# Optimization experiments

Measured on AMD Instinct MI355X. Metric: run time of the kernel, lower is better.

The kernel has to match this reference:

```python
import jax, jax.numpy as jnp
import numpy as np

N, F, O, K = 4096, 128, 128, 4


def setup_inputs() -> dict:
    key = jax.random.key(0)
    ks = jax.random.split(key, 7)
    shift = jax.random.uniform(ks[0], (N, N), jnp.float32) * (1.0 / N)  # dense stand-in for sparse adjacency
    A2 = shift * shift  # elementwise square, as in torch.mul(all_A, all_A)
    x = jax.random.normal(ks[1], (N, F), jnp.float32)
    nan_mask = jax.random.bernoulli(ks[2], 0.1, (N, F))
    features = jnp.where(nan_mask, jnp.nan, x)
    limit = float(np.sqrt(6.0 / (F + O)))  # xavier_uniform
    weight = jax.random.uniform(ks[3], (F, O), jnp.float32, -limit, limit)
    pi = jnp.log(jax.nn.softmax(jax.random.normal(ks[4], (K,), jnp.float32)))  # log mixture weights
    mu = jax.random.normal(ks[5], (K, F), jnp.float32)  # GMM means
    sigma = jnp.log(jax.random.uniform(ks[6], (K, F), jnp.float32, minval=0.5, maxval=1.5))  # log diag covs
    return {"shift": shift, "features": features, "weight": weight,
            "pi": pi, "mu": mu, "sigma": sigma, "A2": A2}


def ex_relu(mu_t, sig_t):
    # E[relu(X)] for X ~ N(mu_t, sig_t), with exact relu fallback when variance == 0
    is_zero = sig_t == 0
    s = jnp.where(is_zero, 1e-10, sig_t)
    sqrt_s = jnp.sqrt(s)
    w = mu_t / sqrt_s
    inv_sqrt_2pi = 1.0 / np.sqrt(2.0 * np.pi)
    nr = sqrt_s * (jnp.exp(-0.5 * w * w) * inv_sqrt_2pi
                   + 0.5 * w * (1.0 + jax.lax.erf(w / np.sqrt(2.0))))
    return jnp.where(is_zero, jnp.maximum(mu_t, 0.0), nr)


def reference(shift, features, weight, pi, mu, sigma, A2):
    dim = features.shape[1]
    x_isnan = jnp.isnan(features)[None, :, :]            # [1, N, F] -> broadcasts over K
    variances = jnp.exp(sigma)                           # [K, F]
    # GMM imputation: mean/variance per component where features missing
    mean_mat = jnp.where(x_isnan, mu[:, None, :], features[None, :, :])      # [K, N, F]
    var_mat = jnp.where(x_isnan, variances[:, None, :], 0.0)                 # [K, N, F]
    # dense GEMMs
    transform_x = jnp.einsum('knf,fo->kno', mean_mat, weight)                # [K, N, O]
    transform_covs = jnp.einsum('knf,fo->kno', var_mat, weight * weight)     # [K, N, O]
    # K graph propagations (spmm in the original)
    conv_x = jnp.einsum('nm,kmo->kno', shift, transform_x)
    conv_covs = jnp.einsum('nm,kmo->kno', A2, transform_covs)
    expected_x = ex_relu(conv_x, conv_covs)                                  # [K, N, O]
    # responsibilities gamma: softmax over components of log pi + log N(x; mu, var)
    log_n = (-0.5 * jnp.sum((mean_mat - mu[:, None, :]) ** 2 / variances[:, None, :], axis=2)
             - 0.5 * dim * np.log(2.0 * np.pi) - 0.5 * jnp.sum(sigma))       # [K, N]
    gamma = jax.nn.softmax(pi[:, None] + log_n, axis=0)                      # [K, N]
    return jnp.sum(expected_x * gamma[:, :, None], axis=0)                   # [N, O]
```

## Files before the change

kernel.cpp:

```cpp
#include <hip/hip_runtime.h>


#define NN 4096
#define FF 128
#define KK 4

typedef _Float16 f16;
typedef f16 f16x8 __attribute__((ext_vector_type(8)));
typedef f16 f16x4 __attribute__((ext_vector_type(4)));
typedef float f32x4 __attribute__((ext_vector_type(4)));

typedef const __attribute__((address_space(1))) void* gptr1_t;
typedef __attribute__((address_space(3))) void* lptr3_t;

__device__ __forceinline__ void gload_lds16(const void* g, void* l) {
  __builtin_amdgcn_global_load_lds((gptr1_t)g, (lptr3_t)l, 16, 0, 0);
}

__device__ __forceinline__ bool is_nan_bits(float x) {
  return (__float_as_uint(x) & 0x7fffffffu) > 0x7f800000u;
}

__global__ __launch_bounds__(256) void k0_prep(
    const float* __restrict__ W, const float* __restrict__ mu,
    const float* __restrict__ sigma, f16* __restrict__ Wx, f16* __restrict__ Wc,
    f16* __restrict__ muh, f16* __restrict__ varh, float* __restrict__ invvar) {
  int tid = blockIdx.x * 256 + threadIdx.x;
  for (int i = tid; i < 16384; i += (int)gridDim.x * 256) {
    int j = i & 7;
    int o = (i >> 3) & 127;
    int g = (i >> 10) & 3;
    int fc = i >> 12;
    int f = fc * 32 + g * 8 + j;
    float w = W[f * 128 + o];
    Wx[i] = (f16)w;
    Wc[i] = (f16)(w * w);
  }
  if (tid < 512) {
    muh[tid] = (f16)mu[tid];
    float s = sigma[tid];
    varh[tid] = (f16)expf(s);
    invvar[tid] = expf(-s);
  }
}

__global__ __launch_bounds__(256) void k1a_gamma(
    const float* __restrict__ feats, const float* __restrict__ mu,
    const float* __restrict__ pi, const float* __restrict__ invvar,
    float* __restrict__ gamma) {
  int wid = threadIdx.x >> 6, lane = threadIdx.x & 63;
  int n = blockIdx.x * 4 + wid;
  const float* rp = feats + (long)n * FF;
  float x0 = rp[lane], x1 = rp[lane + 64];
  bool nan0 = is_nan_bits(x0), nan1 = is_nan_bits(x1);
  float acc[KK];
#pragma unroll
  for (int k = 0; k < KK; ++k) {
    float d0 = x0 - mu[k * FF + lane];
    float d1 = x1 - mu[k * FF + lane + 64];
    float t0 = nan0 ? 0.f : d0 * d0 * invvar[k * FF + lane];
    float t1 = nan1 ? 0.f : d1 * d1 * invvar[k * FF + lane + 64];
    acc[k] = t0 + t1;
  }
#pragma unroll
  for (int off = 32; off > 0; off >>= 1) {
#pragma unroll
    for (int k = 0; k < KK; ++k) acc[k] += __shfl_down(acc[k], off);
  }
  if (lane == 0) {
    float lg[KK], m = -1e30f;
#pragma unroll
    for (int k = 0; k < KK; ++k) {
      lg[k] = pi[k] - 0.5f * acc[k];
      m = fmaxf(m, lg[k]);
    }
    float e[KK], s = 0.f;
#pragma unroll
    for (int k = 0; k < KK; ++k) {
      e[k] = expf(lg[k] - m);
      s += e[k];
    }
    float inv = 1.f / s;
#pragma unroll
    for (int k = 0; k < KK; ++k) gamma[k * NN + n] = e[k] * inv;
  }
}

__global__ __launch_bounds__(256, 2) void k1b_transform(
    const float* __restrict__ feats, const f16* __restrict__ Wx,
    const f16* __restrict__ Wc, const f16* __restrict__ muh,
    const f16* __restrict__ varh, f16* __restrict__ Bws) {
  __shared__ __align__(16) f16 lds[2][4][4][128][8];
  int bid = blockIdx.x;
  int row = bid & 31;
  int kc = bid >> 5;
  int n0 = row * 128;
  int tid = threadIdx.x;
  int wid = tid >> 6, lane = tid & 63;
  int wr = wid >> 1, wc = wid & 1;
  int fr = lane & 15, fg = lane >> 4;
  int sn = tid >> 1, sh = tid & 1;

  f32x4 accx[4][4], accc[4][4];
#pragma unroll
  for (int a = 0; a < 4; ++a)
#pragma unroll
    for (int b = 0; b < 4; ++b) {
      accx[a][b] = f32x4{0.f, 0.f, 0.f, 0.f};
      accc[a][b] = f32x4{0.f, 0.f, 0.f, 0.f};
    }

  const int NT = 4;
  float xs[16];
  f16 mh[16], vh[16];

  auto loadA = [&](int t) {
    const float* ap = feats + (long)(n0 + sn) * FF + t * 32 + sh * 16;
    *(f32x4*)(xs + 0) = *(const f32x4*)(ap + 0);
    *(f32x4*)(xs + 4) = *(const f32x4*)(ap + 4);
    *(f32x4*)(xs + 8) = *(const f32x4*)(ap + 8);
    *(f32x4*)(xs + 12) = *(const f32x4*)(ap + 12);
    const f16* mp = muh + kc * FF + t * 32 + sh * 16;
    const f16* vp = varh + kc * FF + t * 32 + sh * 16;
    *(f16x8*)(mh + 0) = *(const f16x8*)(mp + 0);
    *(f16x8*)(mh + 8) = *(const f16x8*)(mp + 8);
    *(f16x8*)(vh + 0) = *(const f16x8*)(vp + 0);
    *(f16x8*)(vh + 8) = *(const f16x8*)(vp + 8);
  };
  auto writeA = [&](int buf) {
    f16 am[16], av[16];
#pragma unroll
    for (int j = 0; j < 16; ++j) {
      float x = xs[j];
      bool nn = is_nan_bits(x);
      am[j] = nn ? mh[j] : (f16)x;
      av[j] = nn ? vh[j] : (f16)0.f;
    }
    *(f16x8*)&lds[buf][0][2 * sh + 0][sn][0] = *(f16x8*)(am + 0);
    *(f16x8*)&lds[buf][0][2 * sh + 1][sn][0] = *(f16x8*)(am + 8);
    *(f16x8*)&lds[buf][1][2 * sh + 0][sn][0] = *(f16x8*)(av + 0);
    *(f16x8*)&lds[buf][1][2 * sh + 1][sn][0] = *(f16x8*)(av + 8);
  };
  auto stageB = [&](int t, int buf) {
#pragma unroll
    for (int r = 0; r < 2; ++r) {
      int c = r * 256 + tid;
      int cb = r * 256 + wid * 64;
      gload_lds16(Wx + (long)t * 4096 + (long)c * 8, (f16*)&lds[buf][2][0][0][0] + (long)cb * 8);
      gload_lds16(Wc + (long)t * 4096 + (long)c * 8, (f16*)&lds[buf][3][0][0][0] + (long)cb * 8);
    }
  };
  auto compute = [&](int buf) {
    f16x8 am[4], av[4], bx[4], bc[4];
#pragma unroll
    for (int mf = 0; mf < 4; ++mf) {
      am[mf] = *(f16x8*)&lds[buf][0][fg][wr * 64 + mf * 16 + fr][0];
      av[mf] = *(f16x8*)&lds[buf][1][fg][wr * 64 + mf * 16 + fr][0];
    }
#pragma unroll
    for (int nf = 0; nf < 4; ++nf) {
      bx[nf] = *(f16x8*)&lds[buf][2][fg][wc * 64 + nf * 16 + fr][0];
      bc[nf] = *(f16x8*)&lds[buf][3][fg][wc * 64 + nf * 16 + fr][0];
    }
#pragma unroll
    for (int mf = 0; mf < 4; ++mf)
#pragma unroll
      for (int nf = 0; nf < 4; ++nf) {
        accx[mf][nf] = __builtin_amdgcn_mfma_f32_16x16x32_f16(am[mf], bx[nf], accx[mf][nf], 0, 0, 0);
        accc[mf][nf] = __builtin_amdgcn_mfma_f32_16x16x32_f16(av[mf], bc[nf], accc[mf][nf], 0, 0, 0);
      }
  };

  stageB(0, 0);
  loadA(0);
  writeA(0);
  __syncthreads();
  for (int t = 0; t < NT; ++t) {
    int cur = t & 1, nxt = cur ^ 1;
    if (t + 1 < NT) {
      stageB(t + 1, nxt);
      loadA(t + 1);
    }
    compute(cur);
    if (t + 1 < NT) writeA(nxt);
    __syncthreads();
  }

#pragma unroll
  for (int mf = 0; mf < 4; ++mf) {
    int nbase = n0 + wr * 64 + mf * 16 + fg * 4;
#pragma unroll
    for (int nf = 0; nf < 4; ++nf) {
      int col = wc * 64 + nf * 16 + fr;
      f16x4 px, pc;
#pragma unroll
      for (int j = 0; j < 4; ++j) {
        px[j] = (f16)accx[mf][nf][j];
        pc[j] = (f16)accc[mf][nf][j];
      }
      *(f16x4*)(Bws + (long)(kc * 128 + col) * NN + nbase) = px;
      *(f16x4*)(Bws + (long)(512 + kc * 128 + col) * NN + nbase) = pc;
    }
  }
}

__global__ __launch_bounds__(256, 2) void k2_conv(
    const float* __restrict__ shift, const f16* __restrict__ Bws,
    float* __restrict__ convbuf, int mlen) {
  __shared__ __align__(16) f16 lds[2][4][4][128][8];
  int bid = blockIdx.x;
  int row = bid & 31;
  int kc = (bid >> 5) & 3;
  int ks = bid >> 7;
  int n0 = row * 128;
  int m0 = ks * mlen;
  int nt = mlen / 32;
  int tid = threadIdx.x;
  int wid = tid >> 6, lane = tid & 63;
  int wr = wid >> 1, wc = wid & 1;
  int fr = lane & 15, fg = lane >> 4;
  int sn = tid >> 1, sh = tid & 1;

  f32x4 accx[4][4], accc[4][4];
#pragma unroll
  for (int a = 0; a < 4; ++a)
#pragma unroll
    for (int b = 0; b < 4; ++b) {
      accx[a][b] = f32x4{0.f, 0.f, 0.f, 0.f};
      accc[a][b] = f32x4{0.f, 0.f, 0.f, 0.f};
    }

  float xs[16];
  auto loadA = [&](int t) {
    const float* ap = shift + (long)(n0 + sn) * NN + m0 + t * 32 + sh * 16;
    *(f32x4*)(xs + 0) = *(const f32x4*)(ap + 0);
    *(f32x4*)(xs + 4) = *(const f32x4*)(ap + 4);
    *(f32x4*)(xs + 8) = *(const f32x4*)(ap + 8);
    *(f32x4*)(xs + 12) = *(const f32x4*)(ap + 12);
  };
  auto writeA = [&](int buf) {
    f16 sm[16], s2[16];
#pragma unroll
    for (int j = 0; j < 16; ++j) {
      f16 s = (f16)(xs[j] * 4096.f);
      sm[j] = s;
      s2[j] = s * s;
    }
    *(f16x8*)&lds[buf][0][2 * sh + 0][sn][0] = *(f16x8*)(sm + 0);
    *(f16x8*)&lds[buf][0][2 * sh + 1][sn][0] = *(f16x8*)(sm + 8);
    *(f16x8*)&lds[buf][1][2 * sh + 0][sn][0] = *(f16x8*)(s2 + 0);
    *(f16x8*)&lds[buf][1][2 * sh + 1][sn][0] = *(f16x8*)(s2 + 8);
  };
  auto stageB = [&](int t, int buf) {
#pragma unroll
    for (int r = 0; r < 2; ++r) {
      int c = r * 256 + tid;
      int g = c >> 7, col = c & 127;
      int cb = r * 256 + wid * 64;
      const f16* gx = Bws + (long)(kc * 128 + col) * NN + m0 + t * 32 + g * 8;
      const f16* gc = Bws + (long)(512 + kc * 128 + col) * NN + m0 + t * 32 + g * 8;
      gload_lds16(gx, (f16*)&lds[buf][2][0][0][0] + (long)cb * 8);
      gload_lds16(gc, (f16*)&lds[buf][3][0][0][0] + (long)cb * 8);
    }
  };
  auto compute = [&](int buf) {
    f16x8 am[4], av[4], bx[4], bc[4];
#pragma unroll
    for (int mf = 0; mf < 4; ++mf) {
      am[mf] = *(f16x8*)&lds[buf][0][fg][wr * 64 + mf * 16 + fr][0];
      av[mf] = *(f16x8*)&lds[buf][1][fg][wr * 64 + mf * 16 + fr][0];
    }
#pragma unroll
    for (int nf = 0; nf < 4; ++nf) {
      bx[nf] = *(f16x8*)&lds[buf][2][fg][wc * 64 + nf * 16 + fr][0];
      bc[nf] = *(f16x8*)&lds[buf][3][fg][wc * 64 + nf * 16 + fr][0];
    }
#pragma unroll
    for (int mf = 0; mf < 4; ++mf)
#pragma unroll
      for (int nf = 0; nf < 4; ++nf) {
        accx[mf][nf] = __builtin_amdgcn_mfma_f32_16x16x32_f16(am[mf], bx[nf], accx[mf][nf], 0, 0, 0);
        accc[mf][nf] = __builtin_amdgcn_mfma_f32_16x16x32_f16(av[mf], bc[nf], accc[mf][nf], 0, 0, 0);
      }
  };

  stageB(0, 0);
  loadA(0);
  writeA(0);
  __syncthreads();
  for (int t = 0; t < nt; ++t) {
    int cur = t & 1, nxt = cur ^ 1;
    if (t + 1 < nt) {
      stageB(t + 1, nxt);
      loadA(t + 1);
    }
    compute(cur);
    if (t + 1 < nt) writeA(nxt);
    __syncthreads();
  }

  const float sx = 1.f / 4096.f;
  const float sc = 1.f / (4096.f * 4096.f);
  float* base = convbuf + ((long)ks * NN + n0) * 1024;
#pragma unroll
  for (int mf = 0; mf < 4; ++mf) {
#pragma unroll
    for (int nf = 0; nf < 4; ++nf) {
      int o = wc * 64 + nf * 16 + fr;
#pragma unroll
      for (int j = 0; j < 4; ++j) {
        int n = wr * 64 + mf * 16 + fg * 4 + j;
        base[(long)n * 1024 + kc * 128 + o] = accx[mf][nf][j] * sx;
        base[(long)n * 1024 + 512 + kc * 128 + o] = accc[mf][nf][j] * sc;
      }
    }
  }
}

__global__ __launch_bounds__(256) void k3_out(
    const float* __restrict__ convbuf, const float* __restrict__ gamma,
    float* __restrict__ out, int nks) {
  int gid = blockIdx.x * 256 + threadIdx.x;
  int n = gid >> 7, o = gid & 127;
  float cx[KK], cc[KK];
#pragma unroll
  for (int k = 0; k < KK; ++k) {
    cx[k] = 0.f;
    cc[k] = 0.f;
  }
  for (int s = 0; s < nks; ++s) {
    const float* bp = convbuf + ((long)s * NN + n) * 1024;
#pragma unroll
    for (int k = 0; k < KK; ++k) {
      cx[k] += bp[k * 128 + o];
      cc[k] += bp[512 + k * 128 + o];
    }
  }
  const float inv_sqrt_2pi = 0.3989422804014327f;
  float r = 0.f;
#pragma unroll
  for (int k = 0; k < KK; ++k) {
    float s = cc[k];
    bool iz = (s == 0.f);
    float ss = iz ? 1e-10f : s;
    float sq = sqrtf(ss);
    float w = cx[k] / sq;
    float nr = sq * (expf(-0.5f * w * w) * inv_sqrt_2pi +
                     0.5f * w * (1.f + erff(w * 0.7071067811865476f)));
    float ex = iz ? fmaxf(cx[k], 0.f) : nr;
    r += ex * gamma[k * NN + n];
  }
  out[gid] = r;
}

extern "C" void kernel_launch(void* const* d_in, const int* in_sizes, int n_in,
                              void* d_out, int out_size, void* d_ws, size_t ws_size,
                              hipStream_t stream) {
  const float* shift = (const float*)d_in[0];
  const float* feats = (const float*)d_in[1];
  const float* W = (const float*)d_in[2];
  const float* pi = (const float*)d_in[3];
  const float* mu = (const float*)d_in[4];
  const float* sigma = (const float*)d_in[5];
  float* out = (float*)d_out;

  char* w = (char*)d_ws;
  f16* Wx = (f16*)w;        w += 16384 * 2;
  f16* Wc = (f16*)w;        w += 16384 * 2;
  f16* muh = (f16*)w;       w += 512 * 2;
  f16* varh = (f16*)w;      w += 512 * 2;
  float* invvar = (float*)w; w += 512 * 4;
  float* gamma = (float*)w; w += (size_t)KK * NN * 4;
  f16* Bws = (f16*)w;       w += (size_t)1024 * NN * 2;
  float* convbuf = (float*)w;
  size_t used = (size_t)(w - (char*)d_ws);
  size_t slab = (size_t)NN * 1024 * 4;
  int nks = 1;
  if (ws_size >= used + 4 * slab) nks = 4;
  else if (ws_size >= used + 2 * slab) nks = 2;

  hipLaunchKernelGGL(k0_prep, dim3(64), dim3(256), 0, stream, W, mu, sigma, Wx, Wc,
                     muh, varh, invvar);
  hipLaunchKernelGGL(k1a_gamma, dim3(NN / 4), dim3(256), 0, stream, feats, mu, pi,
                     invvar, gamma);
  hipLaunchKernelGGL(k1b_transform, dim3(4 * 32), dim3(256), 0, stream, feats, Wx, Wc,
                     muh, varh, Bws);
  hipLaunchKernelGGL(k2_conv, dim3(nks * 4 * 32), dim3(256), 0, stream, shift, Bws,
                     convbuf, NN / nks);
  hipLaunchKernelGGL(k3_out, dim3(NN * 128 / 256), dim3(256), 0, stream, convbuf,
                     gamma, out, nks);
}
```

Before: 240.9 us.

## Pre-convert shift to fp16 and split conv GEMM into separate mean/cov tiles

Adds a pre-pass that scales and converts the dense fp32 shift matrix to fp16 once into workspace. The conv kernel then streams both A and B through direct global-to-LDS loads, squaring A in registers for covariance tiles. Each block now computes one output tile (mean or cov) with half the accumulators, doubling the grid and allowing higher occupancy. In exchange there is an extra full-matrix read and write pass, and A is re-read by twice as many blocks.

```diff
diff --git a/kernel.cpp b/kernel.cpp
--- a/kernel.cpp
+++ b/kernel.cpp
@@ -44,6 +44,19 @@
   }
 }
 
+__global__ __launch_bounds__(256) void kpre_shift(const float* __restrict__ shift,
+                                                  f16* __restrict__ sh16) {
+  long i = ((long)blockIdx.x * 256 + threadIdx.x) * 8;
+  f32x4 a = *(const f32x4*)(shift + i);
+  f32x4 b = *(const f32x4*)(shift + i + 4);
+  f16x8 o;
+#pragma unroll
+  for (int j = 0; j < 4; ++j) o[j] = (f16)(a[j] * 4096.f);
+#pragma unroll
+  for (int j = 0; j < 4; ++j) o[4 + j] = (f16)(b[j] * 4096.f);
+  *(f16x8*)(sh16 + i) = o;
+}
+
 __global__ __launch_bounds__(256) void k1a_gamma(
     const float* __restrict__ feats, const float* __restrict__ mu,
     const float* __restrict__ pi, const float* __restrict__ invvar,
@@ -204,104 +217,73 @@
   }
 }
 
-__global__ __launch_bounds__(256, 2) void k2_conv(
-    const float* __restrict__ shift, const f16* __restrict__ Bws,
+__global__ __launch_bounds__(256, 4) void k2_conv(
+    const f16* __restrict__ sh16, const f16* __restrict__ Bws,
     float* __restrict__ convbuf, int mlen) {
-  __shared__ __align__(16) f16 lds[2][4][4][128][8];
+  __shared__ __align__(16) f16 la[2][4][128][8];
+  __shared__ __align__(16) f16 lb[2][4][128][8];
   int bid = blockIdx.x;
-  int row = bid & 31;
-  int kc = (bid >> 5) & 3;
-  int ks = bid >> 7;
+  int ct = bid & 7;
+  int row = (bid >> 3) & 31;
+  int ks = bid >> 8;
   int n0 = row * 128;
+  int col0 = ct * 128;
+  bool cov = ct >= 4;
   int m0 = ks * mlen;
   int nt = mlen / 32;
   int tid = threadIdx.x;
   int wid = tid >> 6, lane = tid & 63;
   int wr = wid >> 1, wc = wid & 1;
   int fr = lane & 15, fg = lane >> 4;
-  int sn = tid >> 1, sh = tid & 1;
-
-  f32x4 accx[4][4], accc[4][4];
+
+  f32x4 acc[4][4];
 #pragma unroll
   for (int a = 0; a < 4; ++a)
 #pragma unroll
-    for (int b = 0; b < 4; ++b) {
-      accx[a][b] = f32x4{0.f, 0.f, 0.f, 0.f};
-      accc[a][b] = f32x4{0.f, 0.f, 0.f, 0.f};
-    }
-
-  float xs[16];
-  auto loadA = [&](int t) {
-    const float* ap = shift + (long)(n0 + sn) * NN + m0 + t * 32 + sh * 16;
-    *(f32x4*)(xs + 0) = *(const f32x4*)(ap + 0);
-    *(f32x4*)(xs + 4) = *(const f32x4*)(ap + 4);
-    *(f32x4*)(xs + 8) = *(const f32x4*)(ap + 8);
-    *(f32x4*)(xs + 12) = *(const f32x4*)(ap + 12);
-  };
-  auto writeA = [&](int buf) {
-    f16 sm[16], s2[16];
-#pragma unroll
-    for (int j = 0; j < 16; ++j) {
-      f16 s = (f16)(xs[j] * 4096.f);
-      sm[j] = s;
-      s2[j] = s * s;
-    }
-    *(f16x8*)&lds[buf][0][2 * sh + 0][sn][0] = *(f16x8*)(sm + 0);
-    *(f16x8*)&lds[buf][0][2 * sh + 1][sn][0] = *(f16x8*)(sm + 8);
-    *(f16x8*)&lds[buf][1][2 * sh + 0][sn][0] = *(f16x8*)(s2 + 0);
-    *(f16x8*)&lds[buf][1][2 * sh + 1][sn][0] = *(f16x8*)(s2 + 8);
-  };
-  auto stageB = [&](int t, int buf) {
+    for (int b = 0; b < 4; ++b) acc[a][b] = f32x4{0.f, 0.f, 0.f, 0.f};
+
+  auto stage = [&](int t, int buf) {
 #pragma unroll
     for (int r = 0; r < 2; ++r) {
       int c = r * 256 + tid;
-      int g = c >> 7, col = c & 127;
+      int idx = c & 127, g = c >> 7;
       int cb = r * 256 + wid * 64;
-      const f16* gx = Bws + (long)(kc * 128 + col) * NN + m0 + t * 32 + g * 8;
-      const f16* gc = Bws + (long)(512 + kc * 128 + col) * NN + m0 + t * 32 + g * 8;
-      gload_lds16(gx, (f16*)&lds[buf][2][0][0][0] + (long)cb * 8);
-      gload_lds16(gc, (f16*)&lds[buf][3][0][0][0] + (long)cb * 8);
+      gload_lds16(sh16 + (long)(n0 + idx) * NN + m0 + t * 32 + g * 8,
+                  (f16*)&la[buf][0][0][0] + (long)cb * 8);
+      gload_lds16(Bws + (long)(col0 + idx) * NN + m0 + t * 32 + g * 8,
+                  (f16*)&lb[buf][0][0][0] + (long)cb * 8);
     }
   };
   auto compute = [&](int buf) {
-    f16x8 am[4], av[4], bx[4], bc[4];
-#pragma unroll
-    for (int mf = 0; mf < 4; ++mf) {
-      am[mf] = *(f16x8*)&lds[buf][0][fg][wr * 64 + mf * 16 + fr][0];
-      av[mf] = *(f16x8*)&lds[buf][1][fg][wr * 64 + mf * 16 + fr][0];
-    }
-#pragma unroll
-    for (int nf = 0; nf < 4; ++nf) {
-      bx[nf] = *(f16x8*)&lds[buf][2][fg][wc * 64 + nf * 16 + fr][0];
-      bc[nf] = *(f16x8*)&lds[buf][3][fg][wc * 64 + nf * 16 + fr][0];
-    }
+    f16x8 af[4], bf[4];
 #pragma unroll
     for (int mf = 0; mf < 4; ++mf)
-#pragma unroll
-      for (int nf = 0; nf < 4; ++nf) {
-        accx[mf][nf] = __builtin_amdgcn_mfma_f32_16x16x32_f16(am[mf], bx[nf], accx[mf][nf], 0, 0, 0);
-        accc[mf][nf] = __builtin_amdgcn_mfma_f32_16x16x32_f16(av[mf], bc[nf], accc[mf][nf], 0, 0, 0);
-      }
-  };
-
-  stageB(0, 0);
-  loadA(0);
-  writeA(0);
+      af[mf] = *(f16x8*)&la[buf][fg][wr * 64 + mf * 16 + fr][0];
+#pragma unroll
+    for (int nf = 0; nf < 4; ++nf)
+      bf[nf] = *(f16x8*)&lb[buf][fg][wc * 64 + nf * 16 + fr][0];
+    if (cov) {
+#pragma unroll
+      for (int mf = 0; mf < 4; ++mf) af[mf] = af[mf] * af[mf];
+    }
+#pragma unroll
+    for (int mf = 0; mf < 4; ++mf)
+#pragma unroll
+      for (int nf = 0; nf < 4; ++nf)
+        acc[mf][nf] = __builtin_amdgcn_mfma_f32_16x16x32_f16(af[mf], bf[nf], acc[mf][nf], 0, 0, 0);
+  };
+
+  stage(0, 0);
   __syncthreads();
   for (int t = 0; t < nt; ++t) {
     int cur = t & 1, nxt = cur ^ 1;
-    if (t + 1 < nt) {
-      stageB(t + 1, nxt);
-      loadA(t + 1);
-    }
+    if (t + 1 < nt) stage(t + 1, nxt);
     compute(cur);
-    if (t + 1 < nt) writeA(nxt);
     __syncthreads();
   }
 
-  const float sx = 1.f / 4096.f;
-  const float sc = 1.f / (4096.f * 4096.f);
-  float* base = convbuf + ((long)ks * NN + n0) * 1024;
+  const float dsc = cov ? (1.f / 16777216.f) : (1.f / 4096.f);
+  float* base = convbuf + ((long)ks * NN + n0) * 1024 + col0;
 #pragma unroll
   for (int mf = 0; mf < 4; ++mf) {
 #pragma unroll
@@ -310,8 +292,7 @@
 #pragma unroll
       for (int j = 0; j < 4; ++j) {
         int n = wr * 64 + mf * 16 + fg * 4 + j;
-        base[(long)n * 1024 + kc * 128 + o] = accx[mf][nf][j] * sx;
-        base[(long)n * 1024 + 512 + kc * 128 + o] = accc[mf][nf][j] * sc;
+        base[(long)n * 1024 + o] = acc[mf][nf][j] * dsc;
       }
     }
   }
@@ -372,6 +353,7 @@
   float* invvar = (float*)w; w += 512 * 4;
   float* gamma = (float*)w; w += (size_t)KK * NN * 4;
   f16* Bws = (f16*)w;       w += (size_t)1024 * NN * 2;
+  f16* sh16 = (f16*)w;      w += (size_t)NN * NN * 2;
   float* convbuf = (float*)w;
   size_t used = (size_t)(w - (char*)d_ws);
   size_t slab = (size_t)NN * 1024 * 4;
@@ -381,11 +363,13 @@
 
   hipLaunchKernelGGL(k0_prep, dim3(64), dim3(256), 0, stream, W, mu, sigma, Wx, Wc,
                      muh, varh, invvar);
+  hipLaunchKernelGGL(kpre_shift, dim3((NN * (long)NN) / (256 * 8)), dim3(256), 0,
+                     stream, shift, sh16);
   hipLaunchKernelGGL(k1a_gamma, dim3(NN / 4), dim3(256), 0, stream, feats, mu, pi,
                      invvar, gamma);
   hipLaunchKernelGGL(k1b_transform, dim3(4 * 32), dim3(256), 0, stream, feats, Wx, Wc,
                      muh, varh, Bws);
-  hipLaunchKernelGGL(k2_conv, dim3(nks * 4 * 32), dim3(256), 0, stream, shift, Bws,
+  hipLaunchKernelGGL(k2_conv, dim3(nks * 32 * 8), dim3(256), 0, stream, sh16, Bws,
                      convbuf, NN / nks);
   hipLaunchKernelGGL(k3_out, dim3(NN * 128 / 256), dim3(256), 0, stream, convbuf,
                      gamma, out, nks);
```

Measured after the change: 260.5 us. +8.2%, slower.
